# Kernel optimization log

Hardware: AMD Instinct MI355X
Metric: run time of the kernel (lower is better)

The kernel has to match this reference:

```python
import jax, jax.numpy as jnp
import numpy as np
from jax import lax

# Module constraint: hidden_dim == state_dim == expand_dim (see broadcasting in original).
H = 128  # hidden_dim
N = 128  # state_dim
E = 128  # expand_dim = hidden_dim * expand_factor (expand_factor=1)
B, L = 4, 1024


def setup_inputs() -> dict:
    key = jax.random.key(0)
    ks = jax.random.split(key, 11)
    s = lambda fan: 1.0 / np.sqrt(fan)
    return {
        "u": jax.random.normal(ks[0], (B, L, H), jnp.float32),
        "W_in": jax.random.normal(ks[1], (H, 2 * E), jnp.float32) * s(H),
        "b_in": jax.random.normal(ks[2], (2 * E,), jnp.float32) * 0.01,
        "conv_w": jax.random.normal(ks[3], (E, 1, 3), jnp.float32) * s(3),
        "conv_b": jax.random.normal(ks[4], (E,), jnp.float32) * 0.01,
        "W_x": jax.random.normal(ks[5], (E, N + N + H), jnp.float32) * s(E),
        "b_x": jax.random.normal(ks[6], (N + N + H,), jnp.float32) * 0.01,
        "A_log": jax.random.normal(ks[7], (N,), jnp.float32),
        "D": jnp.ones((H,), jnp.float32),
        "W_out": jax.random.normal(ks[8], (E, H), jnp.float32) * s(E),
        "b_out": jax.random.normal(ks[9], (H,), jnp.float32) * 0.01,
    }


def reference(u, W_in, b_in, conv_w, conv_b, W_x, b_x, A_log, D, W_out, b_out):
    b, l, _ = u.shape
    xz = u @ W_in + b_in                       # [B,L,2E]
    x, z = jnp.split(xz, 2, axis=-1)           # [B,L,E] each
    # depthwise conv1d, kernel 3, padding 1 (groups == channels)
    xc = lax.conv_general_dilated(
        x.transpose(0, 2, 1), conv_w, window_strides=(1,), padding=[(1, 1)],
        feature_group_count=E, dimension_numbers=("NCH", "OIH", "NCH"))
    x = jax.nn.silu(xc.transpose(0, 2, 1) + conv_b)  # [B,L,E]
    ssm = x @ W_x + b_x                        # [B,L,2N+H]
    delta = jax.nn.softplus(ssm[..., :N])      # [B,L,N]
    Bm = ssm[..., N:2 * N]                     # [B,L,N]
    C = ssm[..., 2 * N:]                       # [B,L,H]
    A = -jnp.exp(A_log)                        # [N]

    def step(h, inp):
        d_t, B_t, C_t, x_t, u_t = inp          # [B,N],[B,N],[B,H],[B,E],[B,H]
        # A_discrete[b,t,i,j] = exp(delta[b,t,i] * A[j])  (outer broadcast, as in source)
        A_disc = jnp.exp(d_t[:, :, None] * A[None, None, :])       # [B,N,N]
        h = A_disc * h + (d_t * B_t)[:, :, None] * x_t[:, None, :]  # [B,N,E]
        y = (h * C_t[:, None, :]).sum(axis=1) + D * u_t             # [B,H]
        return h, y

    h0 = jnp.zeros((b, N, H), u.dtype)
    inputs = (delta.transpose(1, 0, 2), Bm.transpose(1, 0, 2),
              C.transpose(1, 0, 2), x.transpose(1, 0, 2), u.transpose(1, 0, 2))
    _, ys = lax.scan(step, h0, inputs)         # ys: [L,B,H]
    y = ys.transpose(1, 0, 2) * jax.nn.silu(z)  # [B,L,H] (E==H)
    return y @ W_out + b_out                   # dropout in eval mode: identity
```

## Files before the change

kernel.cpp:

```cpp
#include <hip/hip_runtime.h>
#include <hip/hip_bf16.h>

using bf16 = __hip_bfloat16;
typedef __attribute__((ext_vector_type(8))) short short8;
typedef __attribute__((ext_vector_type(4))) float f32x4;

#define BVAL 4
#define LVAL 1024
#define LOG2E 1.44269504f

#define TSEG 64
#define SSEG 16
#define JW 8
#define CH 16
#define PTS3 76

#define OFF_U      0
#define OFF_WIN    524288
#define OFF_BIN    557056
#define OFF_CONVW  557312
#define OFF_CONVB  557696
#define OFF_WX     557824
#define OFF_BX     606976
#define OFF_ALOG   607360
#define OFF_D      607488
#define OFF_WOUT   607616
#define OFF_BOUT   624000
#define CVT_TOTAL  624128

__device__ __forceinline__ int dtype_flag(const void* D) {
    return ((*(const unsigned int*)D) & 0xFFFFu) != 0u ? 1 : 0;
}
__device__ __forceinline__ float ldin(const void* p, int i, int f) {
    return f ? __bfloat162float(((const bf16*)p)[i]) : ((const float*)p)[i];
}

__global__ void kcvt(const void* __restrict__ u, const void* __restrict__ W_in,
                     const void* __restrict__ b_in, const void* __restrict__ conv_w,
                     const void* __restrict__ conv_b, const void* __restrict__ W_x,
                     const void* __restrict__ b_x, const void* __restrict__ A_log,
                     const void* __restrict__ D, const void* __restrict__ W_out,
                     const void* __restrict__ b_out, float* __restrict__ dst) {
    int idx = blockIdx.x * 256 + threadIdx.x;
    if (idx >= CVT_TOTAL) return;
    int f = dtype_flag(D);
    const void* p; int loc;
    if      (idx < OFF_WIN)   { p = u;      loc = idx; }
    else if (idx < OFF_BIN)   { p = W_in;   loc = idx - OFF_WIN; }
    else if (idx < OFF_CONVW) { p = b_in;   loc = idx - OFF_BIN; }
    else if (idx < OFF_CONVB) { p = conv_w; loc = idx - OFF_CONVW; }
    else if (idx < OFF_WX)    { p = conv_b; loc = idx - OFF_CONVB; }
    else if (idx < OFF_BX)    { p = W_x;    loc = idx - OFF_WX; }
    else if (idx < OFF_ALOG)  { p = b_x;    loc = idx - OFF_BX; }
    else if (idx < OFF_D)     { p = A_log;  loc = idx - OFF_ALOG; }
    else if (idx < OFF_WOUT)  { p = D;      loc = idx - OFF_D; }
    else if (idx < OFF_BOUT)  { p = W_out;  loc = idx - OFF_WOUT; }
    else                      { p = b_out;  loc = idx - OFF_BOUT; }
    dst[idx] = f ? __bfloat162float(((const bf16*)p)[loc]) : ((const float*)p)[loc];
}

#define CVT2_U   524288
#define CVT2_WI  (CVT2_U + 32768)
#define CVT2_WX  (CVT2_WI + 49152)
#define CVT2_TOT (CVT2_WX + 16384)
__global__ void kcvt2(const void* __restrict__ u, const void* __restrict__ W_in,
                      const void* __restrict__ W_x, const void* __restrict__ W_out,
                      const void* __restrict__ D,
                      bf16* __restrict__ ubf, bf16* __restrict__ wtin,
                      bf16* __restrict__ wtx, bf16* __restrict__ wtout) {
    int idx = blockIdx.x * 256 + threadIdx.x;
    if (idx >= CVT2_TOT) return;
    int f = dtype_flag(D);
    if (idx < CVT2_U) {
        ubf[idx] = __float2bfloat16(ldin(u, idx, f));
    } else if (idx < CVT2_WI) {
        int rel = idx - CVT2_U; int n = rel >> 7, k = rel & 127;
        wtin[rel] = __float2bfloat16(ldin(W_in, k * 256 + n, f));
    } else if (idx < CVT2_WX) {
        int rel = idx - CVT2_WI; int n = rel >> 7, k = rel & 127;
        wtx[rel] = __float2bfloat16(ldin(W_x, k * 384 + n, f));
    } else {
        int rel = idx - CVT2_WX; int n = rel >> 7, k = rel & 127;
        wtout[rel] = __float2bfloat16(ldin(W_out, k * 128 + n, f));
    }
}

__global__ void k1_mfma(const bf16* __restrict__ ubf, const bf16* __restrict__ wtin,
                        const float* __restrict__ cvt,
                        float* __restrict__ x_pre, float* __restrict__ zs) {
    int blk = blockIdx.x, mb = blk >> 3, cb = blk & 7;
    int tid = threadIdx.x, w = tid >> 6, lane = tid & 63;
    int quad = lane >> 4, sub = lane & 15;
    int m0 = mb * 64 + w * 16, c = cb * 16;
    f32x4 accX = {0.f, 0.f, 0.f, 0.f}, accZ = {0.f, 0.f, 0.f, 0.f};
    #pragma unroll
    for (int ks = 0; ks < 4; ++ks) {
        int k0 = ks * 32 + quad * 8;
        short8 a  = *(const short8*)(ubf + (size_t)(m0 + sub) * 128 + k0);
        short8 bX = *(const short8*)(wtin + (size_t)(c + sub) * 128 + k0);
        short8 bZ = *(const short8*)(wtin + (size_t)(128 + c + sub) * 128 + k0);
        accX = __builtin_amdgcn_mfma_f32_16x16x32_bf16(a, bX, accX, 0, 0, 0);
        accZ = __builtin_amdgcn_mfma_f32_16x16x32_bf16(a, bZ, accZ, 0, 0, 0);
    }
    int o = c + sub;
    float bx_ = cvt[OFF_BIN + o], bz_ = cvt[OFF_BIN + 128 + o];
    #pragma unroll
    for (int r = 0; r < 4; ++r) {
        int m = m0 + quad * 4 + r;
        float x = accX[r] + bx_;
        float z = accZ[r] + bz_;
        x_pre[(size_t)m * 128 + o] = x;
        zs[(size_t)m * 128 + o] = z / (1.0f + __expf(-z));
    }
}

__global__ void k2_conv(const float* __restrict__ cvt, const float* __restrict__ x_pre,
                        float* __restrict__ xs, bf16* __restrict__ xsbf) {
    const float* conv_w = cvt + OFF_CONVW;
    const float* conv_b = cvt + OFF_CONVB;
    int q = blockIdx.x * 256 + threadIdx.x;
    int basee = q * 4;
    int row = basee >> 7;
    int l = row & (LVAL - 1);
    int e = basee & 127;
    float4 xc = *(const float4*)(x_pre + basee);
    float4 xm = make_float4(0.f, 0.f, 0.f, 0.f);
    float4 xp = make_float4(0.f, 0.f, 0.f, 0.f);
    if (l > 0)        xm = *(const float4*)(x_pre + basee - 128);
    if (l < LVAL - 1) xp = *(const float4*)(x_pre + basee + 128);
    float mm[4] = {xm.x, xm.y, xm.z, xm.w};
    float cc[4] = {xc.x, xc.y, xc.z, xc.w};
    float pp[4] = {xp.x, xp.y, xp.z, xp.w};
    float out[4];
    #pragma unroll
    for (int i = 0; i < 4; ++i) {
        float w0 = conv_w[(e + i) * 3 + 0];
        float w1 = conv_w[(e + i) * 3 + 1];
        float w2 = conv_w[(e + i) * 3 + 2];
        float v = fmaf(w0, mm[i], fmaf(w1, cc[i], fmaf(w2, pp[i], conv_b[e + i])));
        out[i] = v / (1.0f + __expf(-v));
    }
    *(float4*)(xs + basee) = make_float4(out[0], out[1], out[2], out[3]);
    #pragma unroll
    for (int i = 0; i < 4; ++i) xsbf[basee + i] = __float2bfloat16(out[i]);
}

__global__ void k3_mfma(const bf16* __restrict__ xsbf, const bf16* __restrict__ wtx,
                        const float* __restrict__ cvt,
                        float* __restrict__ delta, float* __restrict__ dB,
                        float* __restrict__ Cc) {
    int blk = blockIdx.x, mb = blk >> 3, cb = blk & 7;
    int tid = threadIdx.x, w = tid >> 6, lane = tid & 63;
    int quad = lane >> 4, sub = lane & 15;
    int m0 = mb * 64 + w * 16, c = cb * 16;
    f32x4 accA = {0.f,0.f,0.f,0.f}, accB = {0.f,0.f,0.f,0.f}, accC = {0.f,0.f,0.f,0.f};
    #pragma unroll
    for (int ks = 0; ks < 4; ++ks) {
        int k0 = ks * 32 + quad * 8;
        short8 a  = *(const short8*)(xsbf + (size_t)(m0 + sub) * 128 + k0);
        short8 bA = *(const short8*)(wtx + (size_t)(c + sub) * 128 + k0);
        short8 bB = *(const short8*)(wtx + (size_t)(128 + c + sub) * 128 + k0);
        short8 bC = *(const short8*)(wtx + (size_t)(256 + c + sub) * 128 + k0);
        accA = __builtin_amdgcn_mfma_f32_16x16x32_bf16(a, bA, accA, 0, 0, 0);
        accB = __builtin_amdgcn_mfma_f32_16x16x32_bf16(a, bB, accB, 0, 0, 0);
        accC = __builtin_amdgcn_mfma_f32_16x16x32_bf16(a, bC, accC, 0, 0, 0);
    }
    int o = c + sub;
    float ba = cvt[OFF_BX + o], bb = cvt[OFF_BX + 128 + o], bc = cvt[OFF_BX + 256 + o];
    #pragma unroll
    for (int r = 0; r < 4; ++r) {
        int m = m0 + quad * 4 + r;
        size_t idx = (size_t)m * 128 + o;
        float d = accA[r] + ba;
        float sp = (d > 20.0f) ? d : log1pf(__expf(d));
        delta[idx] = sp;
        dB[idx] = sp * (accB[r] + bb);
        Cc[idx] = accC[r] + bc;
    }
}

__global__ __launch_bounds__(512, 8)
void k5a(const float* __restrict__ cvt, const float* __restrict__ delta,
         const float* __restrict__ dB, const float* __restrict__ xs,
         float* __restrict__ hout, float* __restrict__ Pout) {
    __shared__ float sdl[CH * 128], swl[CH * 128];
    __shared__ float sx[TSEG][JW];
    int blk = blockIdx.x;
    int b = blk >> 8, s = (blk >> 4) & 15, jg = blk & 15;
    int tid = threadIdx.x, w = tid >> 6, lane = tid & 63;
    int j = jg * JW + w;
    int t0 = s * TSEG;
    size_t base = (size_t)b * LVAL * 128;
    {
        int tt = tid >> 3, jj = tid & 7;
        sx[tt][jj] = xs[base + (size_t)(t0 + tt) * 128 + jg * JW + jj];
    }
    float a2 = -__expf(cvt[OFF_ALOG + j]) * LOG2E;
    float h0 = 0.f, h1 = 0.f, p0 = 1.f, p1 = 1.f;
    const float4* gd4 = (const float4*)(delta + base);
    const float4* gw4 = (const float4*)(dB + base);
    for (int c4 = 0; c4 < TSEG / CH; ++c4) {
        __syncthreads();
        int fb = (t0 + c4 * CH) * 32;
        ((float4*)sdl)[tid] = gd4[fb + tid];
        ((float4*)swl)[tid] = gw4[fb + tid];
        __syncthreads();
        #pragma unroll 8
        for (int k = 0; k < CH; ++k) {
            float2 dd = *(const float2*)&sdl[k * 128 + 2 * lane];
            float2 ww = *(const float2*)&swl[k * 128 + 2 * lane];
            float e0 = exp2f(dd.x * a2), e1 = exp2f(dd.y * a2);
            float xv = sx[c4 * CH + k][w];
            h0 = fmaf(e0, h0, ww.x * xv);
            h1 = fmaf(e1, h1, ww.y * xv);
            p0 *= e0; p1 *= e1;
        }
    }
    size_t cidx = (((size_t)(b * SSEG + s) * 128 + j) * 128) + 2 * lane;
    *(float2*)(hout + cidx) = make_float2(h0, h1);
    *(float2*)(Pout + cidx) = make_float2(p0, p1);
}

__global__ void k5b(const float* __restrict__ hout, const float* __restrict__ Pout,
                    float* __restrict__ hin) {
    int c = blockIdx.x * 2 + (threadIdx.x >> 6);
    int lane = threadIdx.x & 63;
    int b = c >> 7, j = c & 127;
    float h0 = 0.f, h1 = 0.f;
    #pragma unroll
    for (int s = 0; s < SSEG; ++s) {
        size_t idx = (((size_t)(b * SSEG + s) * 128 + j) * 128) + 2 * lane;
        *(float2*)(hin + idx) = make_float2(h0, h1);
        float2 ho = *(const float2*)(hout + idx);
        float2 pp = *(const float2*)(Pout + idx);
        h0 = fmaf(pp.x, h0, ho.x);
        h1 = fmaf(pp.y, h1, ho.y);
    }
}

__global__ __launch_bounds__(512, 8)
void k5c(const float* __restrict__ cvt, const float* __restrict__ delta,
         const float* __restrict__ dB, const float* __restrict__ Cc,
         const float* __restrict__ xs, const float* __restrict__ zs,
         const float* __restrict__ hin, bf16* __restrict__ y2bf) {
    __shared__ float sdl[CH * 128], swl[CH * 128];
    __shared__ float sx[TSEG][JW], sc[TSEG][JW], su[TSEG][JW], sz[TSEG][JW];
    __shared__ float pt[JW][8 * PTS3];
    int blk = blockIdx.x;
    int b = blk >> 8, s = (blk >> 4) & 15, jg = blk & 15;
    int tid = threadIdx.x, w = tid >> 6, lane = tid & 63;
    int j = jg * JW + w;
    int t0 = s * TSEG;
    size_t base = (size_t)b * LVAL * 128;
    {
        int tt = tid >> 3, jj = tid & 7;
        size_t g = base + (size_t)(t0 + tt) * 128 + jg * JW + jj;
        sx[tt][jj] = xs[g];
        sc[tt][jj] = Cc[g];
        su[tt][jj] = cvt[OFF_U + g];
        sz[tt][jj] = zs[g];
    }
    float a2 = -__expf(cvt[OFF_ALOG + j]) * LOG2E;
    float Dj = cvt[OFF_D + j];
    size_t cidx = (((size_t)(b * SSEG + s) * 128 + j) * 128) + 2 * lane;
    float2 hh = *(const float2*)(hin + cidx);
    float h0 = hh.x, h1 = hh.y;
    const float4* gd4 = (const float4*)(delta + base);
    const float4* gw4 = (const float4*)(dB + base);
    float* ptw = pt[w];
    int t_r = lane >> 3, g8 = lane & 7;
    for (int c4 = 0; c4 < TSEG / CH; ++c4) {
        __syncthreads();
        int fb = (t0 + c4 * CH) * 32;
        ((float4*)sdl)[tid] = gd4[fb + tid];
        ((float4*)swl)[tid] = gw4[fb + tid];
        __syncthreads();
        for (int cb = 0; cb < CH / 8; ++cb) {
            #pragma unroll
            for (int k = 0; k < 8; ++k) {
                int kk = cb * 8 + k;
                float2 dd = *(const float2*)&sdl[kk * 128 + 2 * lane];
                float2 ww = *(const float2*)&swl[kk * 128 + 2 * lane];
                float xv = sx[c4 * CH + kk][w];
                h0 = fmaf(exp2f(dd.x * a2), h0, ww.x * xv);
                h1 = fmaf(exp2f(dd.y * a2), h1, ww.y * xv);
                ptw[k * PTS3 + lane] = h0 + h1;
            }
            const float4* pr = (const float4*)&ptw[t_r * PTS3 + g8 * 8];
            float4 v0 = pr[0], v1 = pr[1];
            float sum = ((v0.x + v0.y) + (v0.z + v0.w)) + ((v1.x + v1.y) + (v1.z + v1.w));
            sum += __shfl_xor(sum, 1, 64);
            sum += __shfl_xor(sum, 2, 64);
            sum += __shfl_xor(sum, 4, 64);
            if (g8 == 0) {
                int tt = c4 * CH + cb * 8 + t_r;
                float y = fmaf(sc[tt][w], sum, Dj * su[tt][w]);
                y2bf[base + (size_t)(t0 + tt) * 128 + j] =
                    __float2bfloat16(y * sz[tt][w]);
            }
        }
    }
}

__global__ void k6_mfma(const bf16* __restrict__ y2bf, const bf16* __restrict__ wtout,
                        const float* __restrict__ cvt, const void* __restrict__ Din,
                        void* __restrict__ out) {
    int blk = blockIdx.x, mb = blk >> 2, nb = blk & 3;
    int tid = threadIdx.x, w = tid >> 6, lane = tid & 63;
    int quad = lane >> 4, sub = lane & 15;
    int m0 = mb * 64 + w * 16, n0 = nb * 32;
    f32x4 acc0 = {0.f,0.f,0.f,0.f}, acc1 = {0.f,0.f,0.f,0.f};
    #pragma unroll
    for (int ks = 0; ks < 4; ++ks) {
        int k0 = ks * 32 + quad * 8;
        short8 a  = *(const short8*)(y2bf + (size_t)(m0 + sub) * 128 + k0);
        short8 b0 = *(const short8*)(wtout + (size_t)(n0 + sub) * 128 + k0);
        short8 b1 = *(const short8*)(wtout + (size_t)(n0 + 16 + sub) * 128 + k0);
        acc0 = __builtin_amdgcn_mfma_f32_16x16x32_bf16(a, b0, acc0, 0, 0, 0);
        acc1 = __builtin_amdgcn_mfma_f32_16x16x32_bf16(a, b1, acc1, 0, 0, 0);
    }
    int f = dtype_flag(Din);
    float bo0 = cvt[OFF_BOUT + n0 + sub], bo1 = cvt[OFF_BOUT + n0 + 16 + sub];
    #pragma unroll
    for (int r = 0; r < 4; ++r) {
        int m = m0 + quad * 4 + r;
        float v0 = acc0[r] + bo0, v1 = acc1[r] + bo1;
        if (f) {
            ((bf16*)out)[(size_t)m * 128 + n0 + sub] = __float2bfloat16(v0);
            ((bf16*)out)[(size_t)m * 128 + n0 + 16 + sub] = __float2bfloat16(v1);
        } else {
            ((float*)out)[(size_t)m * 128 + n0 + sub] = v0;
            ((float*)out)[(size_t)m * 128 + n0 + 16 + sub] = v1;
        }
    }
}

extern "C" void kernel_launch(void* const* d_in, const int* in_sizes, int n_in,
                              void* d_out, int out_size, void* d_ws, size_t ws_size,
                              hipStream_t stream) {
    const size_t NE = (size_t)BVAL * LVAL * 128;
    const size_t NC = (size_t)BVAL * SSEG * 128 * 128;

    float* cvt   = (float*)d_ws;
    float* bufs  = cvt + CVT_TOTAL;
    float* x_pre = bufs + 0 * NE;
    float* zs    = bufs + 1 * NE;
    float* xs    = bufs + 2 * NE;
    float* delta = bufs + 3 * NE;
    float* dB    = bufs + 4 * NE;
    float* Cc    = bufs + 5 * NE;
    float* hout  = bufs + 6 * NE;
    float* Pou   = hout + NC;
    float* hin   = Pou + NC;
    float* bfarea = hin + NC;
    bf16* ubf   = (bf16*)bfarea;
    bf16* xsbf  = ubf + NE;
    bf16* y2bf  = xsbf + NE;
    bf16* wtin  = y2bf + NE;
    bf16* wtx   = wtin + 32768;
    bf16* wtout = wtx + 49152;

    const int ROWS = BVAL * LVAL;

    kcvt<<<(CVT_TOTAL + 255) / 256, 256, 0, stream>>>(
        d_in[0], d_in[1], d_in[2], d_in[3], d_in[4], d_in[5],
        d_in[6], d_in[7], d_in[8], d_in[9], d_in[10], cvt);
    kcvt2<<<(CVT2_TOT + 255) / 256, 256, 0, stream>>>(
        d_in[0], d_in[1], d_in[5], d_in[9], d_in[8], ubf, wtin, wtx, wtout);
    k1_mfma<<<512, 256, 0, stream>>>(ubf, wtin, cvt, x_pre, zs);
    k2_conv<<<(ROWS * 128) / (256 * 4), 256, 0, stream>>>(cvt, x_pre, xs, xsbf);
    k3_mfma<<<512, 256, 0, stream>>>(xsbf, wtx, cvt, delta, dB, Cc);
    k5a<<<BVAL * SSEG * (128 / JW), 512, 0, stream>>>(cvt, delta, dB, xs, hout, Pou);
    k5b<<<256, 128, 0, stream>>>(hout, Pou, hin);
    k5c<<<BVAL * SSEG * (128 / JW), 512, 0, stream>>>(cvt, delta, dB, Cc, xs, zs, hin, y2bf);
    k6_mfma<<<256, 256, 0, stream>>>(y2bf, wtout, cvt, d_in[8], d_out);
}
```

Measured before the change: 153.7 us.

## Restructure chunked scan: 8 states per thread, double-buffered LDS, fold carry pass

Merges the two conversion kernels into one launch. Drops the separate k5b carry-propagation kernel, so k5c now rebuilds its incoming state by serially combining all earlier segments' (h, P) pairs. Both scan kernels now use 256-thread blocks covering 16 channels, with each thread holding 8 state elements. The next delta/dB chunk is prefetched into registers and staged into a padded, double-buffered LDS tile, which removes one barrier per chunk. The output reduction now uses shuffles every timestep instead of an LDS partial-sum buffer. The trade-off is redundant carry work that grows with the segment index, more registers per thread, and fewer blocks.

After: 158.1 us. 2.9% more time.

```diff
diff --git a/kernel.cpp b/kernel.cpp
--- a/kernel.cpp
+++ b/kernel.cpp
@@ -11,9 +11,7 @@
 
 #define TSEG 64
 #define SSEG 16
-#define JW 8
-#define CH 16
-#define PTS3 76
+#define RSTR 144
 
 #define OFF_U      0
 #define OFF_WIN    524288
@@ -28,60 +26,57 @@
 #define OFF_BOUT   624000
 #define CVT_TOTAL  624128
 
-__device__ __forceinline__ int dtype_flag(const void* D) {
-    return ((*(const unsigned int*)D) & 0xFFFFu) != 0u ? 1 : 0;
-}
-__device__ __forceinline__ float ldin(const void* p, int i, int f) {
-    return f ? __bfloat162float(((const bf16*)p)[i]) : ((const float*)p)[i];
-}
-
-__global__ void kcvt(const void* __restrict__ u, const void* __restrict__ W_in,
-                     const void* __restrict__ b_in, const void* __restrict__ conv_w,
-                     const void* __restrict__ conv_b, const void* __restrict__ W_x,
-                     const void* __restrict__ b_x, const void* __restrict__ A_log,
-                     const void* __restrict__ D, const void* __restrict__ W_out,
-                     const void* __restrict__ b_out, float* __restrict__ dst) {
-    int idx = blockIdx.x * 256 + threadIdx.x;
-    if (idx >= CVT_TOTAL) return;
-    int f = dtype_flag(D);
-    const void* p; int loc;
-    if      (idx < OFF_WIN)   { p = u;      loc = idx; }
-    else if (idx < OFF_BIN)   { p = W_in;   loc = idx - OFF_WIN; }
-    else if (idx < OFF_CONVW) { p = b_in;   loc = idx - OFF_BIN; }
-    else if (idx < OFF_CONVB) { p = conv_w; loc = idx - OFF_CONVW; }
-    else if (idx < OFF_WX)    { p = conv_b; loc = idx - OFF_CONVB; }
-    else if (idx < OFF_BX)    { p = W_x;    loc = idx - OFF_WX; }
-    else if (idx < OFF_ALOG)  { p = b_x;    loc = idx - OFF_BX; }
-    else if (idx < OFF_D)     { p = A_log;  loc = idx - OFF_ALOG; }
-    else if (idx < OFF_WOUT)  { p = D;      loc = idx - OFF_D; }
-    else if (idx < OFF_BOUT)  { p = W_out;  loc = idx - OFF_WOUT; }
-    else                      { p = b_out;  loc = idx - OFF_BOUT; }
-    dst[idx] = f ? __bfloat162float(((const bf16*)p)[loc]) : ((const float*)p)[loc];
-}
-
 #define CVT2_U   524288
 #define CVT2_WI  (CVT2_U + 32768)
 #define CVT2_WX  (CVT2_WI + 49152)
 #define CVT2_TOT (CVT2_WX + 16384)
-__global__ void kcvt2(const void* __restrict__ u, const void* __restrict__ W_in,
-                      const void* __restrict__ W_x, const void* __restrict__ W_out,
-                      const void* __restrict__ D,
-                      bf16* __restrict__ ubf, bf16* __restrict__ wtin,
-                      bf16* __restrict__ wtx, bf16* __restrict__ wtout) {
+
+__device__ __forceinline__ int dtype_flag(const void* D) {
+    return ((*(const unsigned int*)D) & 0xFFFFu) != 0u ? 1 : 0;
+}
+__device__ __forceinline__ float ldin(const void* p, int i, int f) {
+    return f ? __bfloat162float(((const bf16*)p)[i]) : ((const float*)p)[i];
+}
+
+__global__ void kcvt_all(const void* __restrict__ u, const void* __restrict__ W_in,
+                         const void* __restrict__ b_in, const void* __restrict__ conv_w,
+                         const void* __restrict__ conv_b, const void* __restrict__ W_x,
+                         const void* __restrict__ b_x, const void* __restrict__ A_log,
+                         const void* __restrict__ D, const void* __restrict__ W_out,
+                         const void* __restrict__ b_out, float* __restrict__ dst,
+                         bf16* __restrict__ ubf, bf16* __restrict__ wtin,
+                         bf16* __restrict__ wtx, bf16* __restrict__ wtout) {
     int idx = blockIdx.x * 256 + threadIdx.x;
-    if (idx >= CVT2_TOT) return;
     int f = dtype_flag(D);
-    if (idx < CVT2_U) {
-        ubf[idx] = __float2bfloat16(ldin(u, idx, f));
-    } else if (idx < CVT2_WI) {
-        int rel = idx - CVT2_U; int n = rel >> 7, k = rel & 127;
-        wtin[rel] = __float2bfloat16(ldin(W_in, k * 256 + n, f));
-    } else if (idx < CVT2_WX) {
-        int rel = idx - CVT2_WI; int n = rel >> 7, k = rel & 127;
-        wtx[rel] = __float2bfloat16(ldin(W_x, k * 384 + n, f));
+    if (idx < CVT_TOTAL) {
+        const void* p; int loc;
+        if      (idx < OFF_WIN)   { p = u;      loc = idx; }
+        else if (idx < OFF_BIN)   { p = W_in;   loc = idx - OFF_WIN; }
+        else if (idx < OFF_CONVW) { p = b_in;   loc = idx - OFF_BIN; }
+        else if (idx < OFF_CONVB) { p = conv_w; loc = idx - OFF_CONVW; }
+        else if (idx < OFF_WX)    { p = conv_b; loc = idx - OFF_CONVB; }
+        else if (idx < OFF_BX)    { p = W_x;    loc = idx - OFF_WX; }
+        else if (idx < OFF_ALOG)  { p = b_x;    loc = idx - OFF_BX; }
+        else if (idx < OFF_D)     { p = A_log;  loc = idx - OFF_ALOG; }
+        else if (idx < OFF_WOUT)  { p = D;      loc = idx - OFF_D; }
+        else if (idx < OFF_BOUT)  { p = W_out;  loc = idx - OFF_WOUT; }
+        else                      { p = b_out;  loc = idx - OFF_BOUT; }
+        dst[idx] = ldin(p, loc, f);
     } else {
-        int rel = idx - CVT2_WX; int n = rel >> 7, k = rel & 127;
-        wtout[rel] = __float2bfloat16(ldin(W_out, k * 128 + n, f));
+        int ix = idx - CVT_TOTAL;
+        if (ix >= CVT2_TOT) return;
+        if (ix < CVT2_U) {
+            ubf[ix] = __float2bfloat16(ldin(u, ix, f));
+        } else if (ix < CVT2_WI) {
+            int rel = ix - CVT2_U; int n = rel >> 7, k = rel & 127;
+            wtin[rel] = __float2bfloat16(ldin(W_in, k * 256 + n, f));
+        } else if (ix < CVT2_WX) {
+            int rel = ix - CVT2_WI; int n = rel >> 7, k = rel & 127;
+            wtx[rel] = __float2bfloat16(ldin(W_x, k * 384 + n, f));
+        } else {
+            int rel = ix - CVT2_WX; int n = rel >> 7, k = rel & 127;
+            wtout[rel] = __float2bfloat16(ldin(W_out, k * 128 + n, f));
+        }
     }
 }
 
@@ -179,126 +174,171 @@
     }
 }
 
-__global__ __launch_bounds__(512, 8)
+__device__ __forceinline__ void stage_chunk(float* sdl, float* swl, int tid,
+                                            const float4 rd[2], const float4 rw[2]) {
+    #pragma unroll
+    for (int i = 0; i < 2; ++i) {
+        int q = i * 256 + tid;
+        int t = q >> 5, n4 = q & 31, l = n4 >> 1, hf = n4 & 1;
+        int ad = t * RSTR + 8 * l + 4 * (l >> 2) + 4 * hf;
+        *(float4*)&sdl[ad] = rd[i];
+        *(float4*)&swl[ad] = rw[i];
+    }
+}
+
+__global__ __launch_bounds__(256, 2)
 void k5a(const float* __restrict__ cvt, const float* __restrict__ delta,
          const float* __restrict__ dB, const float* __restrict__ xs,
          float* __restrict__ hout, float* __restrict__ Pout) {
-    __shared__ float sdl[CH * 128], swl[CH * 128];
-    __shared__ float sx[TSEG][JW];
+    __shared__ float sdl[2][16 * RSTR], swl[2][16 * RSTR];
+    __shared__ float sx[TSEG][16];
     int blk = blockIdx.x;
-    int b = blk >> 8, s = (blk >> 4) & 15, jg = blk & 15;
+    int b = blk >> 7, s = (blk >> 3) & 15, jg = blk & 7;
     int tid = threadIdx.x, w = tid >> 6, lane = tid & 63;
-    int j = jg * JW + w;
+    int cj = lane >> 4, ln = lane & 15;
+    int jj = w * 4 + cj, j = jg * 16 + jj;
     int t0 = s * TSEG;
-    size_t base = (size_t)b * LVAL * 128;
+    size_t base = (size_t)b * (LVAL * 128);
     {
-        int tt = tid >> 3, jj = tid & 7;
-        sx[tt][jj] = xs[base + (size_t)(t0 + tt) * 128 + jg * JW + jj];
+        int t = tid >> 2, jc = tid & 3;
+        *(float4*)&sx[t][jc * 4] =
+            *(const float4*)(xs + base + (size_t)(t0 + t) * 128 + jg * 16 + jc * 4);
     }
     float a2 = -__expf(cvt[OFF_ALOG + j]) * LOG2E;
-    float h0 = 0.f, h1 = 0.f, p0 = 1.f, p1 = 1.f;
     const float4* gd4 = (const float4*)(delta + base);
     const float4* gw4 = (const float4*)(dB + base);
-    for (int c4 = 0; c4 < TSEG / CH; ++c4) {
+    float h[8], p[8];
+    #pragma unroll
+    for (int i = 0; i < 8; ++i) { h[i] = 0.f; p[i] = 1.f; }
+    int fb = t0 * 32;
+    float4 rd[2], rw[2];
+    rd[0] = gd4[fb + tid]; rd[1] = gd4[fb + 256 + tid];
+    rw[0] = gw4[fb + tid]; rw[1] = gw4[fb + 256 + tid];
+    stage_chunk(sdl[0], swl[0], tid, rd, rw);
+    __syncthreads();
+    for (int c4 = 0; c4 < 4; ++c4) {
+        if (c4 < 3) {
+            int f2 = fb + (c4 + 1) * 512;
+            rd[0] = gd4[f2 + tid]; rd[1] = gd4[f2 + 256 + tid];
+            rw[0] = gw4[f2 + tid]; rw[1] = gw4[f2 + 256 + tid];
+        }
+        int bf = c4 & 1;
+        int rbase = 8 * ln + 4 * (ln >> 2);
+        #pragma unroll 4
+        for (int k = 0; k < 16; ++k) {
+            int bl = k * RSTR + rbase;
+            float4 d0 = *(const float4*)&sdl[bf][bl];
+            float4 d1 = *(const float4*)&sdl[bf][bl + 4];
+            float4 w0 = *(const float4*)&swl[bf][bl];
+            float4 w1 = *(const float4*)&swl[bf][bl + 4];
+            float xv = sx[c4 * 16 + k][jj];
+            float e;
+            e = exp2f(d0.x * a2); h[0] = fmaf(e, h[0], w0.x * xv); p[0] *= e;
+            e = exp2f(d0.y * a2); h[1] = fmaf(e, h[1], w0.y * xv); p[1] *= e;
+            e = exp2f(d0.z * a2); h[2] = fmaf(e, h[2], w0.z * xv); p[2] *= e;
+            e = exp2f(d0.w * a2); h[3] = fmaf(e, h[3], w0.w * xv); p[3] *= e;
+            e = exp2f(d1.x * a2); h[4] = fmaf(e, h[4], w1.x * xv); p[4] *= e;
+            e = exp2f(d1.y * a2); h[5] = fmaf(e, h[5], w1.y * xv); p[5] *= e;
+            e = exp2f(d1.z * a2); h[6] = fmaf(e, h[6], w1.z * xv); p[6] *= e;
+            e = exp2f(d1.w * a2); h[7] = fmaf(e, h[7], w1.w * xv); p[7] *= e;
+        }
+        if (c4 < 3) stage_chunk(sdl[(c4 + 1) & 1], swl[(c4 + 1) & 1], tid, rd, rw);
         __syncthreads();
-        int fb = (t0 + c4 * CH) * 32;
-        ((float4*)sdl)[tid] = gd4[fb + tid];
-        ((float4*)swl)[tid] = gw4[fb + tid];
-        __syncthreads();
-        #pragma unroll 8
-        for (int k = 0; k < CH; ++k) {
-            float2 dd = *(const float2*)&sdl[k * 128 + 2 * lane];
-            float2 ww = *(const float2*)&swl[k * 128 + 2 * lane];
-            float e0 = exp2f(dd.x * a2), e1 = exp2f(dd.y * a2);
-            float xv = sx[c4 * CH + k][w];
-            h0 = fmaf(e0, h0, ww.x * xv);
-            h1 = fmaf(e1, h1, ww.y * xv);
-            p0 *= e0; p1 *= e1;
-        }
-    }
-    size_t cidx = (((size_t)(b * SSEG + s) * 128 + j) * 128) + 2 * lane;
-    *(float2*)(hout + cidx) = make_float2(h0, h1);
-    *(float2*)(Pout + cidx) = make_float2(p0, p1);
-}
-
-__global__ void k5b(const float* __restrict__ hout, const float* __restrict__ Pout,
-                    float* __restrict__ hin) {
-    int c = blockIdx.x * 2 + (threadIdx.x >> 6);
-    int lane = threadIdx.x & 63;
-    int b = c >> 7, j = c & 127;
-    float h0 = 0.f, h1 = 0.f;
-    #pragma unroll
-    for (int s = 0; s < SSEG; ++s) {
-        size_t idx = (((size_t)(b * SSEG + s) * 128 + j) * 128) + 2 * lane;
-        *(float2*)(hin + idx) = make_float2(h0, h1);
-        float2 ho = *(const float2*)(hout + idx);
-        float2 pp = *(const float2*)(Pout + idx);
-        h0 = fmaf(pp.x, h0, ho.x);
-        h1 = fmaf(pp.y, h1, ho.y);
-    }
-}
-
-__global__ __launch_bounds__(512, 8)
+    }
+    size_t cb = (((size_t)(b * SSEG + s) * 128 + j) * 128) + 8 * ln;
+    *(float4*)(hout + cb)     = make_float4(h[0], h[1], h[2], h[3]);
+    *(float4*)(hout + cb + 4) = make_float4(h[4], h[5], h[6], h[7]);
+    *(float4*)(Pout + cb)     = make_float4(p[0], p[1], p[2], p[3]);
+    *(float4*)(Pout + cb + 4) = make_float4(p[4], p[5], p[6], p[7]);
+}
+
+__global__ __launch_bounds__(256, 2)
 void k5c(const float* __restrict__ cvt, const float* __restrict__ delta,
          const float* __restrict__ dB, const float* __restrict__ Cc,
          const float* __restrict__ xs, const float* __restrict__ zs,
-         const float* __restrict__ hin, bf16* __restrict__ y2bf) {
-    __shared__ float sdl[CH * 128], swl[CH * 128];
-    __shared__ float sx[TSEG][JW], sc[TSEG][JW], su[TSEG][JW], sz[TSEG][JW];
-    __shared__ float pt[JW][8 * PTS3];
+         const float* __restrict__ hout, const float* __restrict__ Pout,
+         bf16* __restrict__ y2bf) {
+    __shared__ float sdl[2][16 * RSTR], swl[2][16 * RSTR];
+    __shared__ float sx[TSEG][16], sc[TSEG][16], su[TSEG][16], sz[TSEG][16];
     int blk = blockIdx.x;
-    int b = blk >> 8, s = (blk >> 4) & 15, jg = blk & 15;
+    int b = blk >> 7, s = (blk >> 3) & 15, jg = blk & 7;
     int tid = threadIdx.x, w = tid >> 6, lane = tid & 63;
-    int j = jg * JW + w;
+    int cj = lane >> 4, ln = lane & 15;
+    int jj = w * 4 + cj, j = jg * 16 + jj;
     int t0 = s * TSEG;
-    size_t base = (size_t)b * LVAL * 128;
+    size_t base = (size_t)b * (LVAL * 128);
     {
-        int tt = tid >> 3, jj = tid & 7;
-        size_t g = base + (size_t)(t0 + tt) * 128 + jg * JW + jj;
-        sx[tt][jj] = xs[g];
-        sc[tt][jj] = Cc[g];
-        su[tt][jj] = cvt[OFF_U + g];
-        sz[tt][jj] = zs[g];
+        int t = tid >> 2, jc = tid & 3;
+        size_t g = base + (size_t)(t0 + t) * 128 + jg * 16 + jc * 4;
+        *(float4*)&sx[t][jc * 4] = *(const float4*)(xs + g);
+        *(float4*)&sc[t][jc * 4] = *(const float4*)(Cc + g);
+        *(float4*)&su[t][jc * 4] = *(const float4*)(cvt + OFF_U + g);
+        *(float4*)&sz[t][jc * 4] = *(const float4*)(zs + g);
     }
     float a2 = -__expf(cvt[OFF_ALOG + j]) * LOG2E;
     float Dj = cvt[OFF_D + j];
-    size_t cidx = (((size_t)(b * SSEG + s) * 128 + j) * 128) + 2 * lane;
-    float2 hh = *(const float2*)(hin + cidx);
-    float h0 = hh.x, h1 = hh.y;
     const float4* gd4 = (const float4*)(delta + base);
     const float4* gw4 = (const float4*)(dB + base);
-    float* ptw = pt[w];
-    int t_r = lane >> 3, g8 = lane & 7;
-    for (int c4 = 0; c4 < TSEG / CH; ++c4) {
+    int fb = t0 * 32;
+    float4 rd[2], rw[2];
+    rd[0] = gd4[fb + tid]; rd[1] = gd4[fb + 256 + tid];
+    rw[0] = gw4[fb + tid]; rw[1] = gw4[fb + 256 + tid];
+    float h[8];
+    #pragma unroll
+    for (int i = 0; i < 8; ++i) h[i] = 0.f;
+    size_t cstep = (size_t)128 * 128;
+    size_t cb0 = (((size_t)(b * SSEG) * 128 + j) * 128) + 8 * ln;
+    for (int sp = 0; sp < s; ++sp) {
+        size_t cb = cb0 + (size_t)sp * cstep;
+        float4 ho0 = *(const float4*)(hout + cb);
+        float4 ho1 = *(const float4*)(hout + cb + 4);
+        float4 pp0 = *(const float4*)(Pout + cb);
+        float4 pp1 = *(const float4*)(Pout + cb + 4);
+        h[0] = fmaf(pp0.x, h[0], ho0.x); h[1] = fmaf(pp0.y, h[1], ho0.y);
+        h[2] = fmaf(pp0.z, h[2], ho0.z); h[3] = fmaf(pp0.w, h[3], ho0.w);
+        h[4] = fmaf(pp1.x, h[4], ho1.x); h[5] = fmaf(pp1.y, h[5], ho1.y);
+        h[6] = fmaf(pp1.z, h[6], ho1.z); h[7] = fmaf(pp1.w, h[7], ho1.w);
+    }
+    stage_chunk(sdl[0], swl[0], tid, rd, rw);
+    __syncthreads();
+    for (int c4 = 0; c4 < 4; ++c4) {
+        if (c4 < 3) {
+            int f2 = fb + (c4 + 1) * 512;
+            rd[0] = gd4[f2 + tid]; rd[1] = gd4[f2 + 256 + tid];
+            rw[0] = gw4[f2 + tid]; rw[1] = gw4[f2 + 256 + tid];
+        }
+        int bf = c4 & 1;
+        int rbase = 8 * ln + 4 * (ln >> 2);
+        #pragma unroll 4
+        for (int k = 0; k < 16; ++k) {
+            int bl = k * RSTR + rbase;
+            float4 d0 = *(const float4*)&sdl[bf][bl];
+            float4 d1 = *(const float4*)&sdl[bf][bl + 4];
+            float4 w0 = *(const float4*)&swl[bf][bl];
+            float4 w1 = *(const float4*)&swl[bf][bl + 4];
+            int t = c4 * 16 + k;
+            float xv = sx[t][jj];
+            float e;
+            e = exp2f(d0.x * a2); h[0] = fmaf(e, h[0], w0.x * xv);
+            e = exp2f(d0.y * a2); h[1] = fmaf(e, h[1], w0.y * xv);
+            e = exp2f(d0.z * a2); h[2] = fmaf(e, h[2], w0.z * xv);
+            e = exp2f(d0.w * a2); h[3] = fmaf(e, h[3], w0.w * xv);
+            e = exp2f(d1.x * a2); h[4] = fmaf(e, h[4], w1.x * xv);
+            e = exp2f(d1.y * a2); h[5] = fmaf(e, h[5], w1.y * xv);
+            e = exp2f(d1.z * a2); h[6] = fmaf(e, h[6], w1.z * xv);
+            e = exp2f(d1.w * a2); h[7] = fmaf(e, h[7], w1.w * xv);
+            float sm = ((h[0] + h[1]) + (h[2] + h[3])) + ((h[4] + h[5]) + (h[6] + h[7]));
+            sm += __shfl_xor(sm, 1, 64);
+            sm += __shfl_xor(sm, 2, 64);
+            sm += __shfl_xor(sm, 4, 64);
+            sm += __shfl_xor(sm, 8, 64);
+            if (ln == 0) {
+                float y = fmaf(sc[t][jj], sm, Dj * su[t][jj]);
+                y2bf[base + (size_t)(t0 + t) * 128 + j] = __float2bfloat16(y * sz[t][jj]);
+            }
+        }
+        if (c4 < 3) stage_chunk(sdl[(c4 + 1) & 1], swl[(c4 + 1) & 1], tid, rd, rw);
         __syncthreads();
-        int fb = (t0 + c4 * CH) * 32;
-        ((float4*)sdl)[tid] = gd4[fb + tid];
-        ((float4*)swl)[tid] = gw4[fb + tid];
-        __syncthreads();
-        for (int cb = 0; cb < CH / 8; ++cb) {
-            #pragma unroll
-            for (int k = 0; k < 8; ++k) {
-                int kk = cb * 8 + k;
-                float2 dd = *(const float2*)&sdl[kk * 128 + 2 * lane];
-                float2 ww = *(const float2*)&swl[kk * 128 + 2 * lane];
-                float xv = sx[c4 * CH + kk][w];
-                h0 = fmaf(exp2f(dd.x * a2), h0, ww.x * xv);
-                h1 = fmaf(exp2f(dd.y * a2), h1, ww.y * xv);
-                ptw[k * PTS3 + lane] = h0 + h1;
-            }
-            const float4* pr = (const float4*)&ptw[t_r * PTS3 + g8 * 8];
-            float4 v0 = pr[0], v1 = pr[1];
-            float sum = ((v0.x + v0.y) + (v0.z + v0.w)) + ((v1.x + v1.y) + (v1.z + v1.w));
-            sum += __shfl_xor(sum, 1, 64);
-            sum += __shfl_xor(sum, 2, 64);
-            sum += __shfl_xor(sum, 4, 64);
-            if (g8 == 0) {
-                int tt = c4 * CH + cb * 8 + t_r;
-                float y = fmaf(sc[tt][w], sum, Dj * su[tt][w]);
-                y2bf[base + (size_t)(t0 + tt) * 128 + j] =
-                    __float2bfloat16(y * sz[tt][w]);
-            }
-        }
     }
 }
 
@@ -351,8 +391,7 @@
     float* Cc    = bufs + 5 * NE;
     float* hout  = bufs + 6 * NE;
     float* Pou   = hout + NC;
-    float* hin   = Pou + NC;
-    float* bfarea = hin + NC;
+    float* bfarea = Pou + NC;
     bf16* ubf   = (bf16*)bfarea;
     bf16* xsbf  = ubf + NE;
     bf16* y2bf  = xsbf + NE;
@@ -361,17 +400,16 @@
     bf16* wtout = wtx + 49152;
 
     const int ROWS = BVAL * LVAL;
-
-    kcvt<<<(CVT_TOTAL + 255) / 256, 256, 0, stream>>>(
+    const int CVT_ALL = CVT_TOTAL + CVT2_TOT;
+
+    kcvt_all<<<(CVT_ALL + 255) / 256, 256, 0, stream>>>(
         d_in[0], d_in[1], d_in[2], d_in[3], d_in[4], d_in[5],
-        d_in[6], d_in[7], d_in[8], d_in[9], d_in[10], cvt);
-    kcvt2<<<(CVT2_TOT + 255) / 256, 256, 0, stream>>>(
-        d_in[0], d_in[1], d_in[5], d_in[9], d_in[8], ubf, wtin, wtx, wtout);
+        d_in[6], d_in[7], d_in[8], d_in[9], d_in[10],
+        cvt, ubf, wtin, wtx, wtout);
     k1_mfma<<<512, 256, 0, stream>>>(ubf, wtin, cvt, x_pre, zs);
     k2_conv<<<(ROWS * 128) / (256 * 4), 256, 0, stream>>>(cvt, x_pre, xs, xsbf);
     k3_mfma<<<512, 256, 0, stream>>>(xsbf, wtx, cvt, delta, dB, Cc);
-    k5a<<<BVAL * SSEG * (128 / JW), 512, 0, stream>>>(cvt, delta, dB, xs, hout, Pou);
-    k5b<<<256, 128, 0, stream>>>(hout, Pou, hin);
-    k5c<<<BVAL * SSEG * (128 / JW), 512, 0, stream>>>(cvt, delta, dB, Cc, xs, zs, hin, y2bf);
+    k5a<<<BVAL * SSEG * 8, 256, 0, stream>>>(cvt, delta, dB, xs, hout, Pou);
+    k5c<<<BVAL * SSEG * 8, 256, 0, stream>>>(cvt, delta, dB, Cc, xs, zs, hout, Pou, y2bf);
     k6_mfma<<<256, 256, 0, stream>>>(y2bf, wtout, cvt, d_in[8], d_out);
 }
```
